# Kernel optimization log

Hardware: AMD Instinct MI355X
Metric: run time of the kernel (lower is better)

Reference implementation:

```python
import jax, jax.numpy as jnp
import numpy as np

B, T = 64, 512
V, F, H = 30000, 256, 256
K = 32          # type_num
PAD, START, END = 0, 30, 31


def make_transition():
    # replicate the exact init order of the torch code
    t = jnp.zeros((K, K), jnp.float32)
    t = t.at[:, START].set(-10000.0)
    t = t.at[END, :].set(-10000.0)
    t = t.at[:, PAD].set(-10000.0)
    t = t.at[PAD, PAD].set(0.0)
    t = t.at[PAD, :END].set(0.0)
    return t


def setup_inputs() -> dict:
    key = jax.random.key(0)
    ks = jax.random.split(key, 12)
    x = jax.random.randint(ks[0], (B, T), 0, V, dtype=jnp.int32)
    tags = jax.random.randint(ks[1], (B, T), 1, START, dtype=jnp.int32)  # real tags, no pad/start/end
    lengths = jax.random.randint(ks[2], (B,), T // 2, T + 1, dtype=jnp.int32)
    mask = (jnp.arange(T, dtype=jnp.int32)[None, :] < lengths[:, None]).astype(jnp.int32)
    s = 0.05
    emb = jax.random.normal(ks[3], (V, F), jnp.float32) * (2.0 / (V + F)) ** 0.5 * 10  # xavier-ish
    w_ih_f = jax.random.normal(ks[4], (4 * H, F), jnp.float32) * s
    w_hh_f = jax.random.normal(ks[5], (4 * H, H), jnp.float32) * s
    b_f = jax.random.normal(ks[6], (4 * H,), jnp.float32) * s  # = b_ih + b_hh (they only ever sum)
    w_ih_b = jax.random.normal(ks[7], (4 * H, F), jnp.float32) * s
    w_hh_b = jax.random.normal(ks[8], (4 * H, H), jnp.float32) * s
    b_b = jax.random.normal(ks[9], (4 * H,), jnp.float32) * s
    w_fc = jax.random.normal(ks[10], (K, 2 * H), jnp.float32) * s
    b_fc = jax.random.normal(ks[11], (K,), jnp.float32) * s
    transition = make_transition()
    return dict(x=x, tags=tags, mask=mask, emb=emb,
                w_ih_f=w_ih_f, w_hh_f=w_hh_f, b_f=b_f,
                w_ih_b=w_ih_b, w_hh_b=w_hh_b, b_b=b_b,
                w_fc=w_fc, b_fc=b_fc, transition=transition)


def _lstm_scan(gx, w_hh):
    # gx: [T, B, 4H] precomputed input gates; PyTorch gate order i, f, g, o
    h0 = jnp.zeros((gx.shape[1], w_hh.shape[1]), gx.dtype)

    def step(carry, g):
        h, c = carry
        z = g + h @ w_hh.T
        i, f, gg, o = jnp.split(z, 4, axis=-1)
        c = jax.nn.sigmoid(f) * c + jax.nn.sigmoid(i) * jnp.tanh(gg)
        h = jax.nn.sigmoid(o) * jnp.tanh(c)
        return (h, c), h

    _, hs = jax.lax.scan(step, (h0, h0), gx)
    return hs  # [T, B, H]


def _crf_loss(scores, tags, mask, transition):
    # scores: [B, T, K], tags/mask: [B, T]
    maskf = mask.astype(scores.dtype)
    b_idx = jnp.arange(scores.shape[0])

    # ---- true path score ----
    first = transition[START, tags[:, 0]] + scores[b_idx, 0, tags[:, 0]]
    tag_sc = jnp.take_along_axis(scores, tags[..., None].astype(jnp.int32), axis=2)[..., 0]  # [B,T]
    tran_sc = transition[tags[:, :-1], tags[:, 1:]]  # [B,T-1]
    body = jnp.sum((tran_sc + tag_sc[:, 1:]) * maskf[:, 1:], axis=1)
    last_idx = jnp.sum(mask, axis=1) - 1
    last_tag = jnp.take_along_axis(tags, last_idx[:, None], axis=1)[:, 0]
    true_prob = first + body + transition[last_tag, END]

    # ---- partition (forward algorithm) via scan ----
    alpha0 = transition[START][None, :] + scores[:, 0]  # [B,K]

    def step(alpha, inp):
        sc, m = inp  # sc: [B,K], m: [B]
        new = jax.nn.logsumexp(alpha[:, :, None] + transition[None, :, :] + sc[:, None, :], axis=1)
        alpha = jnp.where(m[:, None] > 0, new, alpha)
        return alpha, None

    alpha, _ = jax.lax.scan(step, alpha0,
                            (scores.transpose(1, 0, 2)[1:], mask.T[1:]))
    total_prob = jax.nn.logsumexp(alpha + transition[:, END][None, :], axis=1)
    return -jnp.sum(true_prob - total_prob)


def reference(x, tags, mask, emb, w_ih_f, w_hh_f, b_f, w_ih_b, w_hh_b, b_b, w_fc, b_fc, transition):
    e = emb[x]                       # [B,T,F] embedding lookup (dropout = identity, eval mode)
    xt = e.transpose(1, 0, 2)        # [T,B,F]
    # forward direction
    h_f = _lstm_scan(xt @ w_ih_f.T + b_f, w_hh_f)           # [T,B,H]
    # backward direction: reverse time, scan, reverse back
    h_b = _lstm_scan((xt @ w_ih_b.T + b_b)[::-1], w_hh_b)[::-1]
    h = jnp.concatenate([h_f, h_b], axis=-1).transpose(1, 0, 2)  # [B,T,2H]
    scores = h @ w_fc.T + b_fc       # [B,T,K]
    return _crf_loss(scores, tags, mask, transition)
```

## Files before the change

kernel.cpp:

```cpp
#include <hip/hip_runtime.h>

typedef __attribute__((ext_vector_type(8))) short short8;
typedef __attribute__((ext_vector_type(4))) float floatx4;
typedef __attribute__((ext_vector_type(8))) int int8v;

__device__ __forceinline__ float bf2f(unsigned short u) {
    union { unsigned int i; float f; } c; c.i = ((unsigned int)u) << 16; return c.f;
}
__device__ __forceinline__ unsigned short f2bf(float f) {
    union { float f; unsigned int i; } c; c.f = f;
    unsigned int u = c.i;
    return (unsigned short)((u + 0x7FFFu + ((u >> 16) & 1u)) >> 16);
}
__device__ __forceinline__ unsigned short f2bf_rz(float f) {
    union { float f; unsigned int i; } c; c.f = f;
    return (unsigned short)(c.i >> 16);
}
__device__ __forceinline__ float sigm(float x) {
    return __builtin_amdgcn_rcpf(1.f + __expf(-x));
}
__device__ __forceinline__ float tanh_(float x) {
    return 1.f - 2.f * __builtin_amdgcn_rcpf(1.f + __expf(2.f * x));
}

__device__ __forceinline__ void glds16(const void* g, void* l) {
    __builtin_amdgcn_global_load_lds((const __attribute__((address_space(1))) unsigned int*)g,
                                     (__attribute__((address_space(3))) unsigned int*)l, 16, 0, 0);
}

__global__ void k_cast_weights(const float* __restrict__ wihf, const float* __restrict__ wihb,
                               const float* __restrict__ wfc, unsigned short* __restrict__ dst) {
    int i = blockIdx.x * 256 + threadIdx.x;
    if (i >= 532480) return;
    float v;
    if (i < 262144) v = wihf[i];
    else if (i < 524288) v = wihb[i - 262144];
    else v = wfc[i - 524288];
    dst[i] = f2bf(v);
}

__global__ void k_cast_fp8(const float* __restrict__ whhf, const float* __restrict__ whhb,
                           unsigned char* __restrict__ dst) {
    int i = blockIdx.x * 256 + threadIdx.x;
    if (i >= 262144) return;
    int e = i * 2;
    float a = (e < 262144) ? whhf[e] : whhb[e - 262144];
    float b = (e + 1 < 262144) ? whhf[e + 1] : whhb[e + 1 - 262144];
    int p = __builtin_amdgcn_cvt_pk_fp8_f32(a, b, 0, false);
    *(unsigned short*)(dst + e) = (unsigned short)(p & 0xffff);
}

__global__ void k_gather(const int* __restrict__ x, const float* __restrict__ emb,
                         unsigned short* __restrict__ et) {
    int id = blockIdx.x * 256 + threadIdx.x;
    int m = id >> 5, fi = (id & 31) << 3;
    int b = m & 63, t = m >> 6;
    int v = x[b * 512 + t];
    const float4* s = (const float4*)(emb + ((size_t)v << 8) + fi);
    float4 a = s[0], q = s[1];
    uint4 o;
    o.x = (unsigned)f2bf(a.x) | ((unsigned)f2bf(a.y) << 16);
    o.y = (unsigned)f2bf(a.z) | ((unsigned)f2bf(a.w) << 16);
    o.z = (unsigned)f2bf(q.x) | ((unsigned)f2bf(q.y) << 16);
    o.w = (unsigned)f2bf(q.z) | ((unsigned)f2bf(q.w) << 16);
    *(uint4*)(et + ((size_t)m << 8) + fi) = o;
}

__global__ __launch_bounds__(256, 2) void k_gx(const unsigned short* __restrict__ et,
                                               const unsigned short* __restrict__ wcat,
                                               const float* __restrict__ bfv, const float* __restrict__ bbv,
                                               unsigned short* __restrict__ gx) {
    __shared__ unsigned short As[4096];
    __shared__ unsigned short Bs[4096];
    const int tid = threadIdx.x;
    const int w = tid >> 6, l = tid & 63, quad = l >> 4, col = l & 15;
    const size_t m0 = (size_t)blockIdx.x * 128, n0 = (size_t)blockIdx.y * 128;
    floatx4 C[4][4];
    #pragma unroll
    for (int i = 0; i < 4; ++i)
        #pragma unroll
        for (int j = 0; j < 4; ++j) C[i][j] = (floatx4){0.f, 0.f, 0.f, 0.f};
    const int srow = tid >> 2, scol = (tid & 3) * 16;
    for (int it = 0; it < 8; ++it) {
        const char* ga = (const char*)et + (m0 + srow) * 512 + it * 64 + scol;
        const char* gb = (const char*)wcat + (n0 + srow) * 512 + it * 64 + scol;
        glds16(ga,             (char*)As + w * 1024);
        glds16(ga + 64 * 512,  (char*)As + 4096 + w * 1024);
        glds16(gb,             (char*)Bs + w * 1024);
        glds16(gb + 64 * 512,  (char*)Bs + 4096 + w * 1024);
        __syncthreads();
        short8 Af[4], Bf[4];
        #pragma unroll
        for (int i = 0; i < 4; ++i) {
            Af[i] = *(const short8*)(As + (((w & 1) * 64 + i * 16 + col) * 32 + quad * 8));
            Bf[i] = *(const short8*)(Bs + (((w >> 1) * 64 + i * 16 + col) * 32 + quad * 8));
        }
        #pragma unroll
        for (int i = 0; i < 4; ++i)
            #pragma unroll
            for (int j = 0; j < 4; ++j)
                C[i][j] = __builtin_amdgcn_mfma_f32_16x16x32_bf16(Af[i], Bf[j], C[i][j], 0, 0, 0);
        __syncthreads();
    }
    const int mw = (w & 1) * 64, nw = (w >> 1) * 64;
    #pragma unroll
    for (int j = 0; j < 4; ++j) {
        int n = (int)n0 + nw + j * 16 + col;
        float bias = (n < 1024) ? bfv[n] : bbv[n - 1024];
        size_t dbase = (size_t)(n >> 10) * 33554432 + (size_t)(n & 1023);
        #pragma unroll
        for (int i = 0; i < 4; ++i)
            #pragma unroll
            for (int r = 0; r < 4; ++r) {
                size_t m = m0 + mw + i * 16 + quad * 4 + r;
                gx[dbase + m * 1024] = f2bf(C[i][j][r] + bias);
            }
    }
}

__global__ __launch_bounds__(512, 2) void k_lstm(const unsigned char* __restrict__ w8_all,
                                                 const unsigned short* __restrict__ gx_all,
                                                 unsigned short* __restrict__ hcat) {
    const int d = blockIdx.x >> 5, bg = blockIdx.x & 31;
    const int tid = threadIdx.x, w = tid >> 6, l = tid & 63, quad = l >> 4, col = l & 15;
    const unsigned char* W = w8_all + (size_t)d * 262144;
    const unsigned short* G = gx_all + (size_t)d * 33554432;
    __shared__ __align__(16) float zB[2][4][260];
    __shared__ __align__(16) unsigned char hld[2][2][288];

    int8v Wr[4][2][2];
    #pragma unroll
    for (int g = 0; g < 4; ++g)
        #pragma unroll
        for (int ut = 0; ut < 2; ++ut)
            #pragma unroll
            for (int kt = 0; kt < 2; ++kt)
                Wr[g][ut][kt] = *(const int8v*)(W + (size_t)(256 * g + 32 * w + 16 * ut + col) * 256
                                                + kt * 128 + quad * 32);
    for (int i = tid; i < 288; i += 512) ((unsigned int*)hld)[i] = 0;

    const int batch = tid >> 8, j = tid & 255;
    const int bglob = 2 * bg + batch;
    float cst = 0.f;
    const long gstep = d ? -65536 : 65536;
    const long hstep = d ? -32768 : 32768;
    const unsigned short* gp = G + ((size_t)((d ? 511 : 0) * 64 + bglob) * 1024 + j);
    unsigned short* hp = hcat + ((size_t)((d ? 511 : 0) * 64 + bglob) * 512 + d * 256 + j);
    unsigned short gq0 = gp[0], gq1 = gp[256], gq2 = gp[512], gq3 = gp[768];
    gp += gstep;
    __syncthreads();

    #pragma clang loop unroll(disable)
    for (int step = 0; step < 512; ++step) {
        const int cur = step & 1;
        int8v Bf[2];
        #pragma unroll
        for (int kt = 0; kt < 2; ++kt)
            Bf[kt] = *(const int8v*)(&hld[cur][col & 1][kt * 128 + quad * 32]);
        floatx4 C[4][2];
        #pragma unroll
        for (int g = 0; g < 4; ++g)
            #pragma unroll
            for (int ut = 0; ut < 2; ++ut) C[g][ut] = (floatx4){0.f, 0.f, 0.f, 0.f};
        #pragma unroll
        for (int kt = 0; kt < 2; ++kt)
            #pragma unroll
            for (int g = 0; g < 4; ++g)
                #pragma unroll
                for (int ut = 0; ut < 2; ++ut)
                    C[g][ut] = __builtin_amdgcn_mfma_scale_f32_16x16x128_f8f6f4(
                        Wr[g][ut][kt], Bf[kt], C[g][ut], 0, 0, 0, 0x7f7f7f7f, 0, 0x7f7f7f7f);
        if (col < 2) {
            #pragma unroll
            for (int g = 0; g < 4; ++g)
                #pragma unroll
                for (int ut = 0; ut < 2; ++ut)
                    *(floatx4*)(&zB[col][g][32 * w + 16 * ut + 4 * quad]) = C[g][ut];
        }
        __syncthreads();
        float vi = zB[batch][0][j] + bf2f(gq0);
        float vf = zB[batch][1][j] + bf2f(gq1);
        float vg = zB[batch][2][j] + bf2f(gq2);
        float vo = zB[batch][3][j] + bf2f(gq3);
        gq0 = gp[0]; gq1 = gp[256]; gq2 = gp[512]; gq3 = gp[768];
        gp += gstep;
        float cc = sigm(vf) * cst + sigm(vi) * tanh_(vg);
        cst = cc;
        float hf = sigm(vo) * tanh_(cc);
        *hp = f2bf_rz(hf);
        hp += hstep;
        int pk = __builtin_amdgcn_cvt_pk_fp8_f32(hf, hf, 0, false);
        hld[cur ^ 1][batch][j] = (unsigned char)(pk & 0xff);
        __syncthreads();
    }
}

__global__ __launch_bounds__(256, 4) void k_scores(const unsigned short* __restrict__ hcat,
                                                   const unsigned short* __restrict__ wfc,
                                                   const float* __restrict__ bfc,
                                                   float* __restrict__ sc) {
    const int tid = threadIdx.x, w = tid >> 6, l = tid & 63, quad = l >> 4, col = l & 15;
    const int m0 = blockIdx.x * 64 + w * 16;
    floatx4 C0 = (floatx4){0.f, 0.f, 0.f, 0.f}, C1 = C0;
    #pragma unroll
    for (int kt = 0; kt < 16; ++kt) {
        short8 A  = *(const short8*)(hcat + (size_t)(m0 + col) * 512 + kt * 32 + quad * 8);
        short8 B0 = *(const short8*)(wfc + (size_t)col * 512 + kt * 32 + quad * 8);
        short8 B1 = *(const short8*)(wfc + (size_t)(16 + col) * 512 + kt * 32 + quad * 8);
        C0 = __builtin_amdgcn_mfma_f32_16x16x32_bf16(A, B0, C0, 0, 0, 0);
        C1 = __builtin_amdgcn_mfma_f32_16x16x32_bf16(A, B1, C1, 0, 0, 0);
    }
    float b0 = bfc[col], b1 = bfc[16 + col];
    #pragma unroll
    for (int r = 0; r < 4; ++r) {
        int m = m0 + quad * 4 + r;
        sc[(size_t)m * 32 + col] = C0[r] + b0;
        sc[(size_t)m * 32 + 16 + col] = C1[r] + b1;
    }
}

__global__ __launch_bounds__(1024, 1) void k_crf(const float* __restrict__ sc, const int* __restrict__ tags,
                                                 const int* __restrict__ mask, const float* __restrict__ tr,
                                                 float* __restrict__ out) {
    __shared__ float Tm[32][33];
    __shared__ float al[2][32];
    __shared__ float trueb;
    const int b = blockIdx.x, tid = threadIdx.x;
    { int i = tid >> 5, j = tid & 31; Tm[i][j] = tr[tid]; }
    __syncthreads();
    if (tid < 64) {
        float acc = 0.f; int cnt = 0;
        for (int t = tid; t < 512; t += 64) cnt += mask[b * 512 + t];
        for (int t = tid + 1; t < 512; t += 64) {
            if (mask[b * 512 + t]) {
                int tg = tags[b * 512 + t], tp = tags[b * 512 + t - 1];
                acc += Tm[tp][tg] + sc[((size_t)t * 64 + b) * 32 + tg];
            }
        }
        #pragma unroll
        for (int m = 1; m < 64; m <<= 1) { acc += __shfl_xor(acc, m); cnt += __shfl_xor(cnt, m); }
        if (tid == 0) {
            int tg0 = tags[b * 512];
            float first = Tm[30][tg0] + sc[(size_t)b * 32 + tg0];
            int lt = tags[b * 512 + cnt - 1];
            trueb = first + acc + Tm[lt][31];
        }
    }
    if (tid < 32) al[0][tid] = Tm[30][tid] + sc[(size_t)b * 32 + tid];
    __syncthreads();
    const int j = tid >> 5, i = tid & 31;
    int cur = 0;
    float scn = sc[((size_t)64 + b) * 32 + j];
    int mkn = mask[b * 512 + 1];
    #pragma clang loop unroll(disable)
    for (int t = 1; t < 512; ++t) {
        float v = al[cur][i] + Tm[i][j];
        float mx = v;
        #pragma unroll
        for (int m = 1; m < 32; m <<= 1) mx = fmaxf(mx, __shfl_xor(mx, m));
        float e = __expf(v - mx);
        #pragma unroll
        for (int m = 1; m < 32; m <<= 1) e += __shfl_xor(e, m);
        float nv = mx + __logf(e) + scn;
        int mk = mkn;
        int tn = t < 511 ? t + 1 : 511;
        scn = sc[((size_t)tn * 64 + b) * 32 + j];
        mkn = mask[b * 512 + tn];
        if (i == 0) al[cur ^ 1][j] = mk ? nv : al[cur][j];
        __syncthreads();
        cur ^= 1;
    }
    if (tid < 32) {
        float v = al[cur][tid] + Tm[tid][31];
        float mx = v;
        #pragma unroll
        for (int m = 1; m < 32; m <<= 1) mx = fmaxf(mx, __shfl_xor(mx, m));
        float e = __expf(v - mx);
        #pragma unroll
        for (int m = 1; m < 32; m <<= 1) e += __shfl_xor(e, m);
        if (tid == 0) atomicAdd(out, mx + __logf(e) - trueb);
    }
}

extern "C" void kernel_launch(void* const* d_in, const int* in_sizes, int n_in,
                              void* d_out, int out_size, void* d_ws, size_t ws_size,
                              hipStream_t stream) {
    const int* x      = (const int*)d_in[0];
    const int* tags   = (const int*)d_in[1];
    const int* mask   = (const int*)d_in[2];
    const float* emb  = (const float*)d_in[3];
    const float* wihf = (const float*)d_in[4];
    const float* whhf = (const float*)d_in[5];
    const float* bf_  = (const float*)d_in[6];
    const float* wihb = (const float*)d_in[7];
    const float* whhb = (const float*)d_in[8];
    const float* bb_  = (const float*)d_in[9];
    const float* wfc  = (const float*)d_in[10];
    const float* bfc  = (const float*)d_in[11];
    const float* tr   = (const float*)d_in[12];

    char* ws = (char*)d_ws;
    unsigned short* et   = (unsigned short*)(ws);
    unsigned short* wbf  = (unsigned short*)(ws + 16777216);
    unsigned char*  w8   = (unsigned char*)(ws + 17842176);
    unsigned short* gx   = (unsigned short*)(ws + 18366464);
    unsigned short* hcat = (unsigned short*)(ws + 152584192);
    float* sc            = (float*)(ws + 186138624);

    hipMemsetAsync(d_out, 0, sizeof(float), stream);
    k_cast_weights<<<2080, 256, 0, stream>>>(wihf, wihb, wfc, wbf);
    k_cast_fp8<<<1024, 256, 0, stream>>>(whhf, whhb, w8);
    k_gather<<<4096, 256, 0, stream>>>(x, emb, et);
    dim3 g2(256, 16);
    k_gx<<<g2, 256, 0, stream>>>(et, wbf, bf_, bb_, gx);
    k_lstm<<<64, 512, 0, stream>>>(w8, gx, hcat);
    k_scores<<<512, 256, 0, stream>>>(hcat, wbf + 524288, bfc, sc);
    k_crf<<<64, 1024, 0, stream>>>(sc, tags, mask, tr, (float*)d_out);
}
```

Measured before the change: 1.053 ms.

## Swap MFMA operands so gate outputs land in-register, removing zB LDS round-trip

Measured after the change: 915.5 us. -13.1%, faster.

```diff
diff --git a/kernel.cpp b/kernel.cpp
--- a/kernel.cpp
+++ b/kernel.cpp
@@ -125,27 +125,27 @@
     const int tid = threadIdx.x, w = tid >> 6, l = tid & 63, quad = l >> 4, col = l & 15;
     const unsigned char* W = w8_all + (size_t)d * 262144;
     const unsigned short* G = gx_all + (size_t)d * 33554432;
-    __shared__ __align__(16) float zB[2][4][260];
-    __shared__ __align__(16) unsigned char hld[2][2][288];
-
-    int8v Wr[4][2][2];
+    __shared__ __align__(32) unsigned char hld[2][2][288];
+
+    int8v Wb[4][2][2];
     #pragma unroll
     for (int g = 0; g < 4; ++g)
         #pragma unroll
-        for (int ut = 0; ut < 2; ++ut)
+        for (int nt = 0; nt < 2; ++nt)
             #pragma unroll
             for (int kt = 0; kt < 2; ++kt)
-                Wr[g][ut][kt] = *(const int8v*)(W + (size_t)(256 * g + 32 * w + 16 * ut + col) * 256
+                Wb[g][nt][kt] = *(const int8v*)(W + (size_t)(256 * g + 32 * w + 16 * nt + col) * 256
                                                 + kt * 128 + quad * 32);
     for (int i = tid; i < 288; i += 512) ((unsigned int*)hld)[i] = 0;
 
-    const int batch = tid >> 8, j = tid & 255;
-    const int bglob = 2 * bg + batch;
+    const int b = l >> 5, u = 32 * w + (l & 31);
+    const int bglob = 2 * bg + b;
+    const int nts = quad & 1, rs = quad >> 1;
     float cst = 0.f;
     const long gstep = d ? -65536 : 65536;
     const long hstep = d ? -32768 : 32768;
-    const unsigned short* gp = G + ((size_t)((d ? 511 : 0) * 64 + bglob) * 1024 + j);
-    unsigned short* hp = hcat + ((size_t)((d ? 511 : 0) * 64 + bglob) * 512 + d * 256 + j);
+    const unsigned short* gp = G + ((size_t)((d ? 511 : 0) * 64 + bglob) * 1024 + u);
+    unsigned short* hp = hcat + ((size_t)((d ? 511 : 0) * 64 + bglob) * 512 + d * 256 + u);
     unsigned short gq0 = gp[0], gq1 = gp[256], gq2 = gp[512], gq3 = gp[768];
     gp += gstep;
     __syncthreads();
@@ -153,35 +153,40 @@
     #pragma clang loop unroll(disable)
     for (int step = 0; step < 512; ++step) {
         const int cur = step & 1;
-        int8v Bf[2];
+        int8v Af[2];
         #pragma unroll
         for (int kt = 0; kt < 2; ++kt)
-            Bf[kt] = *(const int8v*)(&hld[cur][col & 1][kt * 128 + quad * 32]);
+            Af[kt] = *(const int8v*)(&hld[cur][col & 1][kt * 128 + quad * 32]);
         floatx4 C[4][2];
         #pragma unroll
         for (int g = 0; g < 4; ++g)
             #pragma unroll
-            for (int ut = 0; ut < 2; ++ut) C[g][ut] = (floatx4){0.f, 0.f, 0.f, 0.f};
+            for (int nt = 0; nt < 2; ++nt) C[g][nt] = (floatx4){0.f, 0.f, 0.f, 0.f};
         #pragma unroll
         for (int kt = 0; kt < 2; ++kt)
             #pragma unroll
             for (int g = 0; g < 4; ++g)
                 #pragma unroll
-                for (int ut = 0; ut < 2; ++ut)
-                    C[g][ut] = __builtin_amdgcn_mfma_scale_f32_16x16x128_f8f6f4(
-                        Wr[g][ut][kt], Bf[kt], C[g][ut], 0, 0, 0, 0x7f7f7f7f, 0, 0x7f7f7f7f);
-        if (col < 2) {
-            #pragma unroll
-            for (int g = 0; g < 4; ++g)
-                #pragma unroll
-                for (int ut = 0; ut < 2; ++ut)
-                    *(floatx4*)(&zB[col][g][32 * w + 16 * ut + 4 * quad]) = C[g][ut];
-        }
-        __syncthreads();
-        float vi = zB[batch][0][j] + bf2f(gq0);
-        float vf = zB[batch][1][j] + bf2f(gq1);
-        float vg = zB[batch][2][j] + bf2f(gq2);
-        float vo = zB[batch][3][j] + bf2f(gq3);
+                for (int nt = 0; nt < 2; ++nt)
+                    C[g][nt] = __builtin_amdgcn_mfma_scale_f32_16x16x128_f8f6f4(
+                        Af[kt], Wb[g][nt][kt], C[g][nt], 0, 0, 0, 0x7f7f7f7f, 0, 0x7f7f7f7f);
+        float t0, t1, z0, z1, z2, z3;
+        t0 = nts ? C[0][1][0] : C[0][0][0];
+        t1 = nts ? C[0][1][1] : C[0][0][1];
+        z0 = rs ? t1 : t0;
+        t0 = nts ? C[1][1][0] : C[1][0][0];
+        t1 = nts ? C[1][1][1] : C[1][0][1];
+        z1 = rs ? t1 : t0;
+        t0 = nts ? C[2][1][0] : C[2][0][0];
+        t1 = nts ? C[2][1][1] : C[2][0][1];
+        z2 = rs ? t1 : t0;
+        t0 = nts ? C[3][1][0] : C[3][0][0];
+        t1 = nts ? C[3][1][1] : C[3][0][1];
+        z3 = rs ? t1 : t0;
+        float vi = z0 + bf2f(gq0);
+        float vf = z1 + bf2f(gq1);
+        float vg = z2 + bf2f(gq2);
+        float vo = z3 + bf2f(gq3);
         gq0 = gp[0]; gq1 = gp[256]; gq2 = gp[512]; gq3 = gp[768];
         gp += gstep;
         float cc = sigm(vf) * cst + sigm(vi) * tanh_(vg);
@@ -190,7 +195,7 @@
         *hp = f2bf_rz(hf);
         hp += hstep;
         int pk = __builtin_amdgcn_cvt_pk_fp8_f32(hf, hf, 0, false);
-        hld[cur ^ 1][batch][j] = (unsigned char)(pk & 0xff);
+        hld[cur ^ 1][b][u] = (unsigned char)(pk & 0xff);
         __syncthreads();
     }
 }
```
